# Optimization experiments

Hardware: AMD Instinct MI355X
Metric: run time of the kernel (lower is better)

Reference implementation:

```python
import jax, jax.numpy as jnp
import numpy as np

B, S, NI, NH, NO = 32, 1024, 512, 512, 512


def setup_inputs() -> dict:
    key = jax.random.key(0)
    ks = jax.random.split(key, 6)
    stdv = 1.0 / np.sqrt(NH)
    u = lambda k, shape: jax.random.uniform(k, shape, jnp.float32, -stdv, stdv)
    return {
        "x": jax.random.normal(ks[0], (B, S, NI), jnp.float32),
        "W": u(ks[1], (NI, 4 * NH)),
        "U": u(ks[2], (NH, 4 * NH)),
        "hid_bias": u(ks[3], (4 * NH,)),
        "V": u(ks[4], (NH, NO)),
        "out_bias": u(ks[5], (NO,)),
    }


def reference(x, W, U, hid_bias, V, out_bias):
    B_, S_, _ = x.shape
    nh = U.shape[0]
    # Precompute input contribution for all timesteps: [B,S,4H]
    xW = jnp.einsum("bsi,ih->bsh", x, W) + hid_bias

    def step(carry, xw_t):
        h, c = carry
        gates = xw_t + h @ U  # [B,4H]
        i = jax.nn.sigmoid(gates[:, :nh])
        f = jax.nn.sigmoid(gates[:, nh:2 * nh])
        g = jnp.tanh(gates[:, 2 * nh:3 * nh])
        o = jax.nn.sigmoid(gates[:, 3 * nh:])
        c = f * c + i * g
        h = o * jnp.tanh(c)
        return (h, c), h

    h0 = jnp.zeros((B_, nh), x.dtype)
    c0 = jnp.zeros((B_, nh), x.dtype)
    # scan over time: xW transposed to [S,B,4H]
    _, hidden_seq = jax.lax.scan(step, (h0, c0), jnp.swapaxes(xW, 0, 1))
    hidden_seq = jnp.swapaxes(hidden_seq, 0, 1)  # [B,S,H]
    return jnp.einsum("bsh,ho->bso", hidden_seq, V) + out_bias
```

## Files before the change

kernel.cpp:

```cpp
#include <hip/hip_runtime.h>

typedef unsigned short u16;
typedef unsigned int   u32;

typedef __attribute__((ext_vector_type(8)))  short bf16x8;
typedef __attribute__((ext_vector_type(4)))  float f32x4;
typedef __attribute__((ext_vector_type(8)))  u32   u32x8;
typedef __attribute__((ext_vector_type(16))) float f32x16;

#define B_  32
#define S_  1024
#define NH_ 512
#define G4_ 2048
#define SC_NWG 16
#define CAND  256

__device__ __forceinline__ float bf2f(u16 h) {
    return __uint_as_float(((u32)h) << 16);
}
__device__ __forceinline__ u16 f2bf(float f) {
    u32 u = __float_as_uint(f);
    return (u16)((u + 0x7fffu + ((u >> 16) & 1u)) >> 16);
}
__device__ __forceinline__ float fsig(float x) {
    return 1.0f / (1.0f + __expf(-x));
}
__device__ __forceinline__ float ftanh(float x) {
    return 1.0f - 2.0f / (__expf(2.0f * x) + 1.0f);
}

__global__ void cvt_bf16_kernel(const float* __restrict__ in, u16* __restrict__ out, int n4) {
    int i = blockIdx.x * blockDim.x + threadIdx.x;
    if (i >= n4) return;
    f32x4 v = ((const f32x4*)in)[i];
    unsigned long long pk =
        (unsigned long long)f2bf(v[0]) |
        ((unsigned long long)f2bf(v[1]) << 16) |
        ((unsigned long long)f2bf(v[2]) << 32) |
        ((unsigned long long)f2bf(v[3]) << 48);
    ((unsigned long long*)out)[i] = pk;
}

__global__ void transpose_cvt_kernel(const float* __restrict__ in, u16* __restrict__ out,
                                     int R, int C) {
    __shared__ float tile[32][33];
    int bx = blockIdx.x, by = blockIdx.y;
    int tx = threadIdx.x & 31, ty = threadIdx.x >> 5;
    #pragma unroll
    for (int i = 0; i < 4; i++) {
        int r = by * 32 + ty + i * 8;
        tile[ty + i * 8][tx] = in[(size_t)r * C + bx * 32 + tx];
    }
    __syncthreads();
    #pragma unroll
    for (int i = 0; i < 4; i++) {
        int c = bx * 32 + ty + i * 8;
        out[(size_t)c * R + by * 32 + tx] = f2bf(tile[tx][ty + i * 8]);
    }
}

__global__ __launch_bounds__(256) void gemm_bf16_kernel(
    const u16* __restrict__ A, const u16* __restrict__ BT,
    const float* __restrict__ bias, void* __restrict__ Cp,
    int M, int N, int K, int out_mode)
{
    __shared__ u16 Al[128][40];
    __shared__ u16 Bl[128][40];
    int nbm = M >> 7;
    int bm = blockIdx.x % nbm, bn = blockIdx.x / nbm;
    int tid = threadIdx.x, lane = tid & 63, wave = tid >> 6;
    int wr = wave >> 1, wc = wave & 1;
    f32x4 acc[4][4];
    #pragma unroll
    for (int i = 0; i < 4; i++)
        #pragma unroll
        for (int j = 0; j < 4; j++)
            acc[i][j] = (f32x4){0.f, 0.f, 0.f, 0.f};
    int fr  = lane & 15;
    int kof = (lane >> 4) << 3;

    for (int k0 = 0; k0 < K; k0 += 32) {
        __syncthreads();
        #pragma unroll
        for (int i = 0; i < 2; i++) {
            int chunk = i * 256 + tid;
            int r = chunk >> 2, c = (chunk & 3) << 3;
            *(bf16x8*)&Al[r][c] = *(const bf16x8*)&A[(size_t)(bm * 128 + r) * K + k0 + c];
            *(bf16x8*)&Bl[r][c] = *(const bf16x8*)&BT[(size_t)(bn * 128 + r) * K + k0 + c];
        }
        __syncthreads();
        bf16x8 af[4], bfr[4];
        #pragma unroll
        for (int mi = 0; mi < 4; mi++)
            af[mi] = *(const bf16x8*)&Al[wr * 64 + mi * 16 + fr][kof];
        #pragma unroll
        for (int ni = 0; ni < 4; ni++)
            bfr[ni] = *(const bf16x8*)&Bl[wc * 64 + ni * 16 + fr][kof];
        #pragma unroll
        for (int mi = 0; mi < 4; mi++)
            #pragma unroll
            for (int ni = 0; ni < 4; ni++)
                acc[mi][ni] = __builtin_amdgcn_mfma_f32_16x16x32_bf16(af[mi], bfr[ni], acc[mi][ni], 0, 0, 0);
    }
    int rq = lane >> 4;
    #pragma unroll
    for (int mi = 0; mi < 4; mi++) {
        #pragma unroll
        for (int ni = 0; ni < 4; ni++) {
            int n = bn * 128 + wc * 64 + ni * 16 + fr;
            float bv = bias ? bias[n] : 0.f;
            #pragma unroll
            for (int r = 0; r < 4; r++) {
                int m = bm * 128 + wr * 64 + mi * 16 + rq * 4 + r;
                float v = acc[mi][ni][r] + bv;
                if (out_mode == 1) {
                    int t = m & 1023, b = m >> 10;
                    int g_loc = n >> 9, wg64i = (n >> 3) & 63, u_loc = n & 7;
                    int lane2 = (((b >> 2) & 1) << 5) | (u_loc << 2) | g_loc;
                    int r2 = (b & 3) | ((b >> 3) << 2);
                    ((u16*)Cp)[(((size_t)t * 64 + wg64i) * 64 + lane2) * 16 + r2] = f2bf(v);
                } else {
                    ((float*)Cp)[(size_t)m * N + n] = v;
                }
            }
        }
    }
}

__global__ __launch_bounds__(256, 1) void lstm_scan_kernel(
    const u16* __restrict__ xw,
    const u16* __restrict__ UT,
    u16* __restrict__ hseq,
    u16* __restrict__ hbuf,
    u32* __restrict__ flags,
    u32* __restrict__ elect,
    int* __restrict__ winner)
{
    __shared__ int s_role;
    __shared__ u16 h_lds[32][520];
    __shared__ float gl[4][32][32];
    __shared__ u32 lds_pad[10240];

    const int tid = threadIdx.x;

    lds_pad[tid] = (u32)tid;
    {
        volatile u32* vp = lds_pad;
        u32 dummy = vp[tid];
        asm volatile("" :: "v"(dummy));
    }

    if (tid == 0) {
        u32 xcc;
        asm volatile("s_getreg_b32 %0, hwreg(HW_REG_XCC_ID)" : "=s"(xcc));
        xcc &= 7u;
        u32 r = __hip_atomic_fetch_add(&elect[xcc], 1u,
                    __ATOMIC_ACQ_REL, __HIP_MEMORY_SCOPE_AGENT);
        int role = -1;
        if (r < (u32)SC_NWG) {
            if (r == (u32)SC_NWG - 1) {
                int expv = -1;
                __hip_atomic_compare_exchange_strong(winner, &expv, (int)xcc,
                    __ATOMIC_ACQ_REL, __ATOMIC_ACQUIRE, __HIP_MEMORY_SCOPE_AGENT);
            }
            int w = -1;
            for (int spins = 0; spins < 200000; spins++) {
                w = __hip_atomic_load(winner, __ATOMIC_ACQUIRE,
                                      __HIP_MEMORY_SCOPE_AGENT);
                if (w >= 0) break;
                __builtin_amdgcn_s_sleep(8);
            }
            role = (w == (int)xcc) ? (int)r : -1;
        }
        s_role = role;
    }
    __syncthreads();
    const int role = s_role;
    if (role < 0) return;

    const int wave = tid >> 6, lane = tid & 63;
    const int wg64 = role * 4 + wave;
    const int col  = lane & 31, half = lane >> 5;
    const int u_loc = col >> 2, g_loc = col & 3;
    const int ucol  = g_loc * 512 + wg64 * 8 + u_loc;

    bf16x8 ufrag[32];
    {
        const u16* ub = &UT[(size_t)ucol * 512 + half * 8];
        #define LDU4(i0)                                                      \
            asm volatile(                                                     \
                "global_load_dwordx4 %0, %4, off\n\t"                         \
                "global_load_dwordx4 %1, %4, off offset:32\n\t"               \
                "global_load_dwordx4 %2, %4, off offset:64\n\t"               \
                "global_load_dwordx4 %3, %4, off offset:96"                   \
                : "=&v"(ufrag[i0]), "=&v"(ufrag[i0 + 1]),                     \
                  "=&v"(ufrag[i0 + 2]), "=&v"(ufrag[i0 + 3])                  \
                : "v"(ub + (i0) * 16))
        LDU4(0); LDU4(4); LDU4(8); LDU4(12);
        LDU4(16); LDU4(20); LDU4(24); LDU4(28);
        #undef LDU4
        asm volatile("s_waitcnt vmcnt(0)" ::: "memory");
    }

    float cst[4] = {0.f, 0.f, 0.f, 0.f};

    {
        bf16x8 z = (bf16x8){0, 0, 0, 0, 0, 0, 0, 0};
        bf16x8* hf = (bf16x8*)&h_lds[0][0];
        for (int i = tid; i < 2080; i += 256) hf[i] = z;
    }

    const int sb_b  = tid >> 4;
    const int sb_ic = tid & 15;

    for (int t = 0; t < 1024; t++) {
        const u16* xp = xw + ((size_t)((size_t)t * 64 + wg64) * 64 + lane) * 16;
        bf16x8 xv0 = *(const bf16x8*)xp;
        bf16x8 xv1 = *(const bf16x8*)(xp + 8);

        if (t > 0) {
            const u32 tg = (u32)t;
            {
                u32x8 f0, f1;
                int rounds = 0;
                while (1) {
                    asm volatile("s_dcache_inv\n\t"
                                 "s_load_dwordx8 %0, %2, 0x0\n\t"
                                 "s_load_dwordx8 %1, %2, 0x20\n\t"
                                 "s_waitcnt lgkmcnt(0)"
                                 : "=s"(f0), "=s"(f1) : "s"(flags) : "memory");
                    bool ok = f0[0] >= tg && f0[1] >= tg && f0[2] >= tg &&
                              f0[3] >= tg && f0[4] >= tg && f0[5] >= tg &&
                              f0[6] >= tg && f0[7] >= tg &&
                              f1[0] >= tg && f1[1] >= tg && f1[2] >= tg &&
                              f1[3] >= tg && f1[4] >= tg && f1[5] >= tg &&
                              f1[6] >= tg && f1[7] >= tg;
                    if (ok || ++rounds > (1 << 13)) break;
                }
            }
            asm volatile("buffer_inv" ::: "memory");
            const char* sb0 = (const char*)(hbuf + ((size_t)(t & 1) << 14))
                              + sb_b * 1024 + sb_ic * 16;
            f32x4 r0, r1, r2, r3, r4, r5, r6, r7;
            asm volatile(
                "global_load_dwordx4 %0, %8, off\n\t"
                "global_load_dwordx4 %1, %8, off offset:256\n\t"
                "global_load_dwordx4 %2, %8, off offset:512\n\t"
                "global_load_dwordx4 %3, %8, off offset:768\n\t"
                "global_load_dwordx4 %4, %9, off\n\t"
                "global_load_dwordx4 %5, %9, off offset:256\n\t"
                "global_load_dwordx4 %6, %9, off offset:512\n\t"
                "global_load_dwordx4 %7, %9, off offset:768\n\t"
                "s_waitcnt vmcnt(0)"
                : "=&v"(r0), "=&v"(r1), "=&v"(r2), "=&v"(r3),
                  "=&v"(r4), "=&v"(r5), "=&v"(r6), "=&v"(r7)
                : "v"(sb0), "v"(sb0 + 16384) : "memory");
            __builtin_amdgcn_sched_barrier(0);
            u16* d0 = &h_lds[sb_b][sb_ic * 8];
            u16* d1 = &h_lds[sb_b + 16][sb_ic * 8];
            *(f32x4*)(d0)       = r0;
            *(f32x4*)(d0 + 128) = r1;
            *(f32x4*)(d0 + 256) = r2;
            *(f32x4*)(d0 + 384) = r3;
            *(f32x4*)(d1)       = r4;
            *(f32x4*)(d1 + 128) = r5;
            *(f32x4*)(d1 + 256) = r6;
            *(f32x4*)(d1 + 384) = r7;
        }
        __syncthreads();

        f32x16 a0 = {0,0,0,0, 0,0,0,0, 0,0,0,0, 0,0,0,0};
        f32x16 a1 = {0,0,0,0, 0,0,0,0, 0,0,0,0, 0,0,0,0};
        #pragma unroll
        for (int kk = 0; kk < 16; kk++) {
            bf16x8 af0 = *(const bf16x8*)&h_lds[col][kk * 16 + half * 8];
            a0 = __builtin_amdgcn_mfma_f32_32x32x16_bf16(af0, ufrag[kk], a0, 0, 0, 0);
            bf16x8 af1 = *(const bf16x8*)&h_lds[col][(kk + 16) * 16 + half * 8];
            a1 = __builtin_amdgcn_mfma_f32_32x32x16_bf16(af1, ufrag[kk + 16], a1, 0, 0, 0);
        }

        #pragma unroll
        for (int r = 0; r < 16; r++) {
            int b = (r & 3) + ((r >> 2) << 3) + (half << 2);
            float xwv = bf2f(r < 8 ? (u16)xv0[r] : (u16)xv1[r - 8]);
            gl[wave][b][col] = a0[r] + a1[r] + xwv;
        }

        u16 hv[4];
        int bi[4];
        #pragma unroll
        for (int i = 0; i < 4; i++) {
            int p = (i << 6) + lane, b = p >> 3, u = p & 7;
            f32x4 g4 = *(const f32x4*)&gl[wave][b][u << 2];
            float si = fsig(g4[0]), sf = fsig(g4[1]);
            float sg = ftanh(g4[2]), so = fsig(g4[3]);
            float c = sf * cst[i] + si * sg;
            cst[i] = c;
            hv[i] = f2bf(so * ftanh(c));
            bi[i] = b;
        }
        u16* hb_out = hbuf + ((size_t)(((size_t)t + 1) & 1) << 14);
        const int j = (wg64 << 3);
        #pragma unroll
        for (int i = 0; i < 4; i++) {
            int p = (i << 6) + lane, u = p & 7;
            u32 hw = hv[i];
            u16* hp = hb_out + bi[i] * 512 + j + u;
            asm volatile("global_store_short %0, %1, off"
                         :: "v"(hp), "v"(hw) : "memory");
        }
        asm volatile("s_waitcnt vmcnt(0)" ::: "memory");
        __syncthreads();
        if (tid == 0) {
            u32 fv = (u32)(t + 1);
            u32* fq = flags + role;
            asm volatile("global_store_dword %0, %1, off"
                         :: "v"(fq), "v"(fv) : "memory");
        }
        #pragma unroll
        for (int i = 0; i < 4; i++) {
            int p = (i << 6) + lane, u = p & 7;
            hseq[((size_t)bi[i] * S_ + t) * NH_ + j + u] = hv[i];
        }
    }
}

extern "C" void kernel_launch(void* const* d_in, const int* in_sizes, int n_in,
                              void* d_out, int out_size, void* d_ws, size_t ws_size,
                              hipStream_t stream) {
    const float* x        = (const float*)d_in[0];
    const float* W        = (const float*)d_in[1];
    const float* U        = (const float*)d_in[2];
    const float* hid_bias = (const float*)d_in[3];
    const float* V        = (const float*)d_in[4];
    const float* out_bias = (const float*)d_in[5];

    char* ws = (char*)d_ws;
    size_t off = 0;
    auto carve = [&](size_t bytes) -> void* {
        void* p = ws + off;
        off += (bytes + 255) & ~(size_t)255;
        return p;
    };
    u16* xw     = (u16*)carve((size_t)B_ * S_ * G4_ * 2);
    u16* xbf    = (u16*)carve((size_t)B_ * S_ * NH_ * 2);
    u16* hseq   = (u16*)carve((size_t)B_ * S_ * NH_ * 2);
    u16* WT     = (u16*)carve((size_t)G4_ * NH_ * 2);
    u16* UT     = (u16*)carve((size_t)G4_ * NH_ * 2);
    u16* VT     = (u16*)carve((size_t)NH_ * NH_ * 2);
    u16* hbuf   = (u16*)carve((size_t)2 * B_ * NH_ * 2);
    u32* flags  = (u32*)carve(256);
    u32* elect  = (u32*)carve(256);
    int* winner = (int*)carve(256);

    hipMemsetAsync(flags, 0, 256, stream);
    hipMemsetAsync(elect, 0, 256, stream);
    hipMemsetAsync(winner, 0xFF, 256, stream);

    int n4 = B_ * S_ * NH_ / 4;
    cvt_bf16_kernel<<<(n4 + 255) / 256, 256, 0, stream>>>(x, xbf, n4);
    transpose_cvt_kernel<<<dim3(G4_ / 32, NH_ / 32), 256, 0, stream>>>(W, WT, NH_, G4_);
    transpose_cvt_kernel<<<dim3(G4_ / 32, NH_ / 32), 256, 0, stream>>>(U, UT, NH_, G4_);
    transpose_cvt_kernel<<<dim3(NH_ / 32, NH_ / 32), 256, 0, stream>>>(V, VT, NH_, NH_);

    gemm_bf16_kernel<<<4096, 256, 0, stream>>>(xbf, WT, hid_bias, xw,
                                               B_ * S_, G4_, NH_, 1);
    lstm_scan_kernel<<<CAND, 256, 0, stream>>>(xw, UT, hseq, hbuf,
                                               flags, elect, winner);
    gemm_bf16_kernel<<<1024, 256, 0, stream>>>(hseq, VT, out_bias, d_out,
                                               B_ * S_, NH_, NH_, 0);
}
```

Measured before the change: 3.244 ms.

## Split LSTM scan across 32 workgroups of two waves each

Halves the workgroup size of the persistent LSTM scan kernel from four waves to two and doubles the number of cooperating workgroups from 16 to 32, so each workgroup owns fewer hidden units. The flag poll now checks 32 flags, and each thread stages the hidden state into LDS in two load batches instead of one. The intent is to spread the recurrent matmul over more compute units and cut per-step latency, at the cost of more cross-workgroup synchronization traffic and a longer flag check each timestep.

```diff
diff --git a/kernel.cpp b/kernel.cpp
--- a/kernel.cpp
+++ b/kernel.cpp
@@ -12,7 +12,7 @@
 #define S_  1024
 #define NH_ 512
 #define G4_ 2048
-#define SC_NWG 16
+#define SC_NWG 32
 #define CAND  256
 
 __device__ __forceinline__ float bf2f(u16 h) {
@@ -127,7 +127,7 @@
     }
 }
 
-__global__ __launch_bounds__(256, 1) void lstm_scan_kernel(
+__global__ __launch_bounds__(128, 1) void lstm_scan_kernel(
     const u16* __restrict__ xw,
     const u16* __restrict__ UT,
     u16* __restrict__ hseq,
@@ -138,7 +138,7 @@
 {
     __shared__ int s_role;
     __shared__ u16 h_lds[32][520];
-    __shared__ float gl[4][32][32];
+    __shared__ float gl[2][32][32];
     __shared__ u32 lds_pad[10240];
 
     const int tid = threadIdx.x;
@@ -179,7 +179,7 @@
     if (role < 0) return;
 
     const int wave = tid >> 6, lane = tid & 63;
-    const int wg64 = role * 4 + wave;
+    const int wg64 = role * 2 + wave;
     const int col  = lane & 31, half = lane >> 5;
     const int u_loc = col >> 2, g_loc = col & 3;
     const int ucol  = g_loc * 512 + wg64 * 8 + u_loc;
@@ -207,7 +207,7 @@
     {
         bf16x8 z = (bf16x8){0, 0, 0, 0, 0, 0, 0, 0};
         bf16x8* hf = (bf16x8*)&h_lds[0][0];
-        for (int i = tid; i < 2080; i += 256) hf[i] = z;
+        for (int i = tid; i < 2080; i += 128) hf[i] = z;
     }
 
     const int sb_b  = tid >> 4;
@@ -221,20 +221,23 @@
         if (t > 0) {
             const u32 tg = (u32)t;
             {
-                u32x8 f0, f1;
+                u32x8 f0, f1, f2, f3;
                 int rounds = 0;
                 while (1) {
                     asm volatile("s_dcache_inv\n\t"
-                                 "s_load_dwordx8 %0, %2, 0x0\n\t"
-                                 "s_load_dwordx8 %1, %2, 0x20\n\t"
+                                 "s_load_dwordx8 %0, %4, 0x0\n\t"
+                                 "s_load_dwordx8 %1, %4, 0x20\n\t"
+                                 "s_load_dwordx8 %2, %4, 0x40\n\t"
+                                 "s_load_dwordx8 %3, %4, 0x60\n\t"
                                  "s_waitcnt lgkmcnt(0)"
-                                 : "=s"(f0), "=s"(f1) : "s"(flags) : "memory");
-                    bool ok = f0[0] >= tg && f0[1] >= tg && f0[2] >= tg &&
-                              f0[3] >= tg && f0[4] >= tg && f0[5] >= tg &&
-                              f0[6] >= tg && f0[7] >= tg &&
-                              f1[0] >= tg && f1[1] >= tg && f1[2] >= tg &&
-                              f1[3] >= tg && f1[4] >= tg && f1[5] >= tg &&
-                              f1[6] >= tg && f1[7] >= tg;
+                                 : "=s"(f0), "=s"(f1), "=s"(f2), "=s"(f3)
+                                 : "s"(flags) : "memory");
+                    bool ok = true;
+                    #pragma unroll
+                    for (int q = 0; q < 8; q++) {
+                        ok = ok && f0[q] >= tg && f1[q] >= tg &&
+                                   f2[q] >= tg && f3[q] >= tg;
+                    }
                     if (ok || ++rounds > (1 << 13)) break;
                 }
             }
@@ -254,18 +257,37 @@
                 "s_waitcnt vmcnt(0)"
                 : "=&v"(r0), "=&v"(r1), "=&v"(r2), "=&v"(r3),
                   "=&v"(r4), "=&v"(r5), "=&v"(r6), "=&v"(r7)
-                : "v"(sb0), "v"(sb0 + 16384) : "memory");
+                : "v"(sb0), "v"(sb0 + 8192) : "memory");
+            {
+                u16* d0 = &h_lds[sb_b][sb_ic * 8];
+                u16* d1 = &h_lds[sb_b + 8][sb_ic * 8];
+                *(f32x4*)(d0) = r0; *(f32x4*)(d0 + 128) = r1;
+                *(f32x4*)(d0 + 256) = r2; *(f32x4*)(d0 + 384) = r3;
+                *(f32x4*)(d1) = r4; *(f32x4*)(d1 + 128) = r5;
+                *(f32x4*)(d1 + 256) = r6; *(f32x4*)(d1 + 384) = r7;
+            }
+            asm volatile(
+                "global_load_dwordx4 %0, %8, off\n\t"
+                "global_load_dwordx4 %1, %8, off offset:256\n\t"
+                "global_load_dwordx4 %2, %8, off offset:512\n\t"
+                "global_load_dwordx4 %3, %8, off offset:768\n\t"
+                "global_load_dwordx4 %4, %9, off\n\t"
+                "global_load_dwordx4 %5, %9, off offset:256\n\t"
+                "global_load_dwordx4 %6, %9, off offset:512\n\t"
+                "global_load_dwordx4 %7, %9, off offset:768\n\t"
+                "s_waitcnt vmcnt(0)"
+                : "=&v"(r0), "=&v"(r1), "=&v"(r2), "=&v"(r3),
+                  "=&v"(r4), "=&v"(r5), "=&v"(r6), "=&v"(r7)
+                : "v"(sb0 + 16384), "v"(sb0 + 24576) : "memory");
             __builtin_amdgcn_sched_barrier(0);
-            u16* d0 = &h_lds[sb_b][sb_ic * 8];
-            u16* d1 = &h_lds[sb_b + 16][sb_ic * 8];
-            *(f32x4*)(d0)       = r0;
-            *(f32x4*)(d0 + 128) = r1;
-            *(f32x4*)(d0 + 256) = r2;
-            *(f32x4*)(d0 + 384) = r3;
-            *(f32x4*)(d1)       = r4;
-            *(f32x4*)(d1 + 128) = r5;
-            *(f32x4*)(d1 + 256) = r6;
-            *(f32x4*)(d1 + 384) = r7;
+            {
+                u16* d2 = &h_lds[sb_b + 16][sb_ic * 8];
+                u16* d3 = &h_lds[sb_b + 24][sb_ic * 8];
+                *(f32x4*)(d2) = r0; *(f32x4*)(d2 + 128) = r1;
+                *(f32x4*)(d2 + 256) = r2; *(f32x4*)(d2 + 384) = r3;
+                *(f32x4*)(d3) = r4; *(f32x4*)(d3 + 128) = r5;
+                *(f32x4*)(d3 + 256) = r6; *(f32x4*)(d3 + 384) = r7;
+            }
         }
         __syncthreads();
 
@@ -365,7 +387,7 @@
 
     gemm_bf16_kernel<<<4096, 256, 0, stream>>>(xbf, WT, hid_bias, xw,
                                                B_ * S_, G4_, NH_, 1);
-    lstm_scan_kernel<<<CAND, 256, 0, stream>>>(xw, UT, hseq, hbuf,
+    lstm_scan_kernel<<<CAND, 128, 0, stream>>>(xw, UT, hseq, hbuf,
                                                flags, elect, winner);
     gemm_bf16_kernel<<<1024, 256, 0, stream>>>(hseq, VT, out_bias, d_out,
                                                B_ * S_, NH_, NH_, 0);
```

Result: slower. 3.325 ms (+2.5%).

## Pad per-workgroup flags to separate lines and prefetch next-step xW during scan

Applied to the files above, without the earlier changes.

Each workgroup's step flag now lives on its own 64-byte slot instead of sharing one packed region, so the 16 flag writers no longer contend on the same cache line. Pollers read them with 16 scalar loads. The next timestep's xW gates are loaded at the end of each iteration so that latency overlaps the barrier spin, and buffer_inv moves before the polling loop. Risks: moving the invalidate before the spin may leave stale hbuf data visible, and the prefetch on the last step reads one step past the end of xW.

```diff
diff --git a/kernel.cpp b/kernel.cpp
--- a/kernel.cpp
+++ b/kernel.cpp
@@ -5,7 +5,6 @@
 
 typedef __attribute__((ext_vector_type(8)))  short bf16x8;
 typedef __attribute__((ext_vector_type(4)))  float f32x4;
-typedef __attribute__((ext_vector_type(8)))  u32   u32x8;
 typedef __attribute__((ext_vector_type(16))) float f32x16;
 
 #define B_  32
@@ -213,32 +212,55 @@
     const int sb_b  = tid >> 4;
     const int sb_ic = tid & 15;
 
+    bf16x8 xv0, xv1;
+    {
+        const u16* xp0 = xw + ((size_t)wg64 * 64 + lane) * 16;
+        asm volatile("global_load_dwordx4 %0, %2, off\n\t"
+                     "global_load_dwordx4 %1, %2, off offset:16\n\t"
+                     "s_waitcnt vmcnt(0)"
+                     : "=&v"(xv0), "=&v"(xv1) : "v"(xp0) : "memory");
+    }
+
     for (int t = 0; t < 1024; t++) {
-        const u16* xp = xw + ((size_t)((size_t)t * 64 + wg64) * 64 + lane) * 16;
-        bf16x8 xv0 = *(const bf16x8*)xp;
-        bf16x8 xv1 = *(const bf16x8*)(xp + 8);
-
         if (t > 0) {
             const u32 tg = (u32)t;
+            asm volatile("buffer_inv" ::: "memory");
             {
-                u32x8 f0, f1;
+                u32 f0, f1, f2, f3, f4, f5, f6, f7;
+                u32 f8, f9, fa, fb, fc, fd, fe, ff;
                 int rounds = 0;
                 while (1) {
-                    asm volatile("s_dcache_inv\n\t"
-                                 "s_load_dwordx8 %0, %2, 0x0\n\t"
-                                 "s_load_dwordx8 %1, %2, 0x20\n\t"
-                                 "s_waitcnt lgkmcnt(0)"
-                                 : "=s"(f0), "=s"(f1) : "s"(flags) : "memory");
-                    bool ok = f0[0] >= tg && f0[1] >= tg && f0[2] >= tg &&
-                              f0[3] >= tg && f0[4] >= tg && f0[5] >= tg &&
-                              f0[6] >= tg && f0[7] >= tg &&
-                              f1[0] >= tg && f1[1] >= tg && f1[2] >= tg &&
-                              f1[3] >= tg && f1[4] >= tg && f1[5] >= tg &&
-                              f1[6] >= tg && f1[7] >= tg;
+                    asm volatile(
+                        "s_dcache_inv\n\t"
+                        "s_load_dword %0, %16, 0x0\n\t"
+                        "s_load_dword %1, %16, 0x40\n\t"
+                        "s_load_dword %2, %16, 0x80\n\t"
+                        "s_load_dword %3, %16, 0xC0\n\t"
+                        "s_load_dword %4, %16, 0x100\n\t"
+                        "s_load_dword %5, %16, 0x140\n\t"
+                        "s_load_dword %6, %16, 0x180\n\t"
+                        "s_load_dword %7, %16, 0x1C0\n\t"
+                        "s_load_dword %8, %16, 0x200\n\t"
+                        "s_load_dword %9, %16, 0x240\n\t"
+                        "s_load_dword %10, %16, 0x280\n\t"
+                        "s_load_dword %11, %16, 0x2C0\n\t"
+                        "s_load_dword %12, %16, 0x300\n\t"
+                        "s_load_dword %13, %16, 0x340\n\t"
+                        "s_load_dword %14, %16, 0x380\n\t"
+                        "s_load_dword %15, %16, 0x3C0\n\t"
+                        "s_waitcnt lgkmcnt(0)"
+                        : "=s"(f0), "=s"(f1), "=s"(f2), "=s"(f3),
+                          "=s"(f4), "=s"(f5), "=s"(f6), "=s"(f7),
+                          "=s"(f8), "=s"(f9), "=s"(fa), "=s"(fb),
+                          "=s"(fc), "=s"(fd), "=s"(fe), "=s"(ff)
+                        : "s"(flags) : "memory");
+                    bool ok = f0 >= tg && f1 >= tg && f2 >= tg && f3 >= tg &&
+                              f4 >= tg && f5 >= tg && f6 >= tg && f7 >= tg &&
+                              f8 >= tg && f9 >= tg && fa >= tg && fb >= tg &&
+                              fc >= tg && fd >= tg && fe >= tg && ff >= tg;
                     if (ok || ++rounds > (1 << 13)) break;
                 }
             }
-            asm volatile("buffer_inv" ::: "memory");
             const char* sb0 = (const char*)(hbuf + ((size_t)(t & 1) << 14))
                               + sb_b * 1024 + sb_ic * 16;
             f32x4 r0, r1, r2, r3, r4, r5, r6, r7;
@@ -313,7 +335,7 @@
         __syncthreads();
         if (tid == 0) {
             u32 fv = (u32)(t + 1);
-            u32* fq = flags + role;
+            u32* fq = flags + role * 16;
             asm volatile("global_store_dword %0, %1, off"
                          :: "v"(fq), "v"(fv) : "memory");
         }
@@ -321,6 +343,12 @@
         for (int i = 0; i < 4; i++) {
             int p = (i << 6) + lane, u = p & 7;
             hseq[((size_t)bi[i] * S_ + t) * NH_ + j + u] = hv[i];
+        }
+        {
+            const u16* xpn = xw + (((size_t)(t + 1) * 64 + wg64) * 64 + lane) * 16;
+            asm volatile("global_load_dwordx4 %0, %2, off\n\t"
+                         "global_load_dwordx4 %1, %2, off offset:16"
+                         : "=&v"(xv0), "=&v"(xv1) : "v"(xpn) : "memory");
         }
     }
 }
@@ -349,11 +377,11 @@
     u16* UT     = (u16*)carve((size_t)G4_ * NH_ * 2);
     u16* VT     = (u16*)carve((size_t)NH_ * NH_ * 2);
     u16* hbuf   = (u16*)carve((size_t)2 * B_ * NH_ * 2);
-    u32* flags  = (u32*)carve(256);
+    u32* flags  = (u32*)carve(1024);
     u32* elect  = (u32*)carve(256);
     int* winner = (int*)carve(256);
 
-    hipMemsetAsync(flags, 0, 256, stream);
+    hipMemsetAsync(flags, 0, 1024, stream);
     hipMemsetAsync(elect, 0, 256, stream);
     hipMemsetAsync(winner, 0xFF, 256, stream);
 
```

Result: slower. 3.314 ms (+2.2%).

## Reorder x rows time-major, pack xW stores, and load GEMM tiles directly to LDS

Applied to the files above, without the earlier changes.

The bf16 conversion of x now writes rows in time-major (s,b) order, so GEMM output rows map to consecutive batch entries per timestep. The xW epilogue can then pack four bf16 gate values into one 64-bit store into the scan's swizzled layout instead of scattered 16-bit stores. GEMM tile loads use global_load_lds, which writes global memory straight into LDS without a register round trip, and the LDS padding is removed. Dropping the padding may add LDS bank conflicts on the fragment reads, and the row reordering must stay consistent with the scan's indexing.

```diff
diff --git a/kernel.cpp b/kernel.cpp
--- a/kernel.cpp
+++ b/kernel.cpp
@@ -2,6 +2,7 @@
 
 typedef unsigned short u16;
 typedef unsigned int   u32;
+typedef unsigned long long u64;
 
 typedef __attribute__((ext_vector_type(8)))  short bf16x8;
 typedef __attribute__((ext_vector_type(4)))  float f32x4;
@@ -33,12 +34,15 @@
     int i = blockIdx.x * blockDim.x + threadIdx.x;
     if (i >= n4) return;
     f32x4 v = ((const f32x4*)in)[i];
-    unsigned long long pk =
-        (unsigned long long)f2bf(v[0]) |
-        ((unsigned long long)f2bf(v[1]) << 16) |
-        ((unsigned long long)f2bf(v[2]) << 32) |
-        ((unsigned long long)f2bf(v[3]) << 48);
-    ((unsigned long long*)out)[i] = pk;
+    u64 pk =
+        (u64)f2bf(v[0]) |
+        ((u64)f2bf(v[1]) << 16) |
+        ((u64)f2bf(v[2]) << 32) |
+        ((u64)f2bf(v[3]) << 48);
+    int c4 = i & 127;
+    int s  = (i >> 7) & 1023;
+    int b  = i >> 17;
+    ((u64*)out)[((size_t)(s * 32 + b)) * 128 + c4] = pk;
 }
 
 __global__ void transpose_cvt_kernel(const float* __restrict__ in, u16* __restrict__ out,
@@ -64,8 +68,8 @@
     const float* __restrict__ bias, void* __restrict__ Cp,
     int M, int N, int K, int out_mode)
 {
-    __shared__ u16 Al[128][40];
-    __shared__ u16 Bl[128][40];
+    __shared__ u16 Al[128][32];
+    __shared__ u16 Bl[128][32];
     int nbm = M >> 7;
     int bm = blockIdx.x % nbm, bn = blockIdx.x / nbm;
     int tid = threadIdx.x, lane = tid & 63, wave = tid >> 6;
@@ -85,8 +89,14 @@
         for (int i = 0; i < 2; i++) {
             int chunk = i * 256 + tid;
             int r = chunk >> 2, c = (chunk & 3) << 3;
-            *(bf16x8*)&Al[r][c] = *(const bf16x8*)&A[(size_t)(bm * 128 + r) * K + k0 + c];
-            *(bf16x8*)&Bl[r][c] = *(const bf16x8*)&BT[(size_t)(bn * 128 + r) * K + k0 + c];
+            __builtin_amdgcn_global_load_lds(
+                (const __attribute__((address_space(1))) u32*)
+                    &A[(size_t)(bm * 128 + r) * K + k0 + c],
+                (__attribute__((address_space(3))) u32*)&Al[r][c], 16, 0, 0);
+            __builtin_amdgcn_global_load_lds(
+                (const __attribute__((address_space(1))) u32*)
+                    &BT[(size_t)(bn * 128 + r) * K + k0 + c],
+                (__attribute__((address_space(3))) u32*)&Bl[r][c], 16, 0, 0);
         }
         __syncthreads();
         bf16x8 af[4], bfr[4];
@@ -103,24 +113,36 @@
                 acc[mi][ni] = __builtin_amdgcn_mfma_f32_16x16x32_bf16(af[mi], bfr[ni], acc[mi][ni], 0, 0, 0);
     }
     int rq = lane >> 4;
-    #pragma unroll
-    for (int mi = 0; mi < 4; mi++) {
-        #pragma unroll
-        for (int ni = 0; ni < 4; ni++) {
-            int n = bn * 128 + wc * 64 + ni * 16 + fr;
-            float bv = bias ? bias[n] : 0.f;
+    if (out_mode == 1) {
+        #pragma unroll
+        for (int mi = 0; mi < 4; mi++) {
+            int m0 = bm * 128 + wr * 64 + mi * 16 + rq * 4;
+            int t  = m0 >> 5, B0 = m0 & 31;
             #pragma unroll
-            for (int r = 0; r < 4; r++) {
-                int m = bm * 128 + wr * 64 + mi * 16 + rq * 4 + r;
-                float v = acc[mi][ni][r] + bv;
-                if (out_mode == 1) {
-                    int t = m & 1023, b = m >> 10;
-                    int g_loc = n >> 9, wg64i = (n >> 3) & 63, u_loc = n & 7;
-                    int lane2 = (((b >> 2) & 1) << 5) | (u_loc << 2) | g_loc;
-                    int r2 = (b & 3) | ((b >> 3) << 2);
-                    ((u16*)Cp)[(((size_t)t * 64 + wg64i) * 64 + lane2) * 16 + r2] = f2bf(v);
-                } else {
-                    ((float*)Cp)[(size_t)m * N + n] = v;
+            for (int ni = 0; ni < 4; ni++) {
+                int n = bn * 128 + wc * 64 + ni * 16 + fr;
+                float bv = bias[n];
+                int g_loc = n >> 9, wg64i = (n >> 3) & 63, u_loc = n & 7;
+                int lane2 = (((B0 >> 2) & 1) << 5) | (u_loc << 2) | g_loc;
+                u64 pk =
+                    (u64)f2bf(acc[mi][ni][0] + bv) |
+                    ((u64)f2bf(acc[mi][ni][1] + bv) << 16) |
+                    ((u64)f2bf(acc[mi][ni][2] + bv) << 32) |
+                    ((u64)f2bf(acc[mi][ni][3] + bv) << 48);
+                ((u64*)Cp)[(((size_t)t * 64 + wg64i) * 64 + lane2) * 4 + (B0 >> 3)] = pk;
+            }
+        }
+    } else {
+        #pragma unroll
+        for (int mi = 0; mi < 4; mi++) {
+            #pragma unroll
+            for (int ni = 0; ni < 4; ni++) {
+                int n = bn * 128 + wc * 64 + ni * 16 + fr;
+                float bv = bias ? bias[n] : 0.f;
+                #pragma unroll
+                for (int r = 0; r < 4; r++) {
+                    int m = bm * 128 + wr * 64 + mi * 16 + rq * 4 + r;
+                    ((float*)Cp)[(size_t)m * N + n] = acc[mi][ni][r] + bv;
                 }
             }
         }
```

After: 2.826 ms. 1.15x faster.
